# Optimization experiments

Hardware: AMD Instinct MI355X
Metric: run time of the kernel (lower is better)

The kernel has to match this reference:

```python
import jax, jax.numpy as jnp
import numpy as np

B, S, D, H = 4, 1024, 512, 8
DH = D // H
INNER = 1536  # int(2*D*4/3) rounded up to multiple of 256


def setup_inputs() -> dict:
    key = jax.random.key(0)
    ks = jax.random.split(key, 16)
    g = lambda i, shape, fan: (jax.random.normal(ks[i], shape, jnp.float32) / np.sqrt(fan))
    return {
        "x": jax.random.normal(ks[0], (B, S, D), jnp.float32),
        "Wq": g(1, (D, D), D), "bq": jnp.zeros((D,), jnp.float32),
        "Wkv": g(2, (D, 2 * D), D), "bkv": jnp.zeros((2 * D,), jnp.float32),
        "Wo": g(3, (D, D), D), "bo": jnp.zeros((D,), jnp.float32),
        "rms_w": jnp.ones((D,), jnp.float32),
        "l1": g(4, (D, INNER), D), "l2": g(5, (D, INNER), D), "l3": g(6, (INNER, D), INNER),
        "in_w": jnp.ones((D,), jnp.float32), "in_b": jnp.zeros((D,), jnp.float32),
    }


def rms_norm(x, w, eps=1e-6):
    return x * jax.lax.rsqrt(jnp.mean(x * x, axis=-1, keepdims=True) + eps) * w


def instance_norm(x, w, b, eps=1e-5):
    # InstanceNorm1d(affine=True) over the sequence dim per (batch, channel); x: [B,S,D]
    m = jnp.mean(x, axis=1, keepdims=True)
    v = jnp.mean((x - m) ** 2, axis=1, keepdims=True)
    return (x - m) * jax.lax.rsqrt(v + eps) * w + b


def sparse_sdpa(q, k, v):
    # q,k,v: [B,H,S,DH]
    b, h, s, dh = q.shape
    scores = jnp.einsum("bhsd,bhtd->bhst", q, k) / np.sqrt(dh).astype(np.float32)
    w = jax.nn.softmax(scores, axis=-1)
    kk = s // 2
    _, idx = jax.lax.top_k(w, kk)  # [B,H,S,kk]
    bi = jnp.arange(b)[:, None, None, None]
    hi = jnp.arange(h)[None, :, None, None]
    ri = jnp.arange(s)[None, None, :, None]
    mask = jnp.zeros_like(w).at[bi, hi, ri, idx].set(1.0)
    masked = jnp.where(mask > 0, w, 0.0)  # zeros (not -inf), per original
    aw = jax.nn.softmax(masked, axis=-1)
    return jnp.einsum("bhst,bhtd->bhsd", aw, v)


def reference(x, Wq, bq, Wkv, bkv, Wo, bo, rms_w, l1, l2, l3, in_w, in_b):
    # attention: q from Wq, k/v from packed Wkv ('b s (two h d)')
    q = (x @ Wq + bq).reshape(B, S, H, DH).transpose(0, 2, 1, 3)
    kv = (x @ Wkv + bkv).reshape(B, S, 2, H, DH)
    k = kv[:, :, 0].transpose(0, 2, 1, 3)
    v = kv[:, :, 1].transpose(0, 2, 1, 3)
    o = sparse_sdpa(q, k, v)
    attn_out = o.transpose(0, 2, 1, 3).reshape(B, S, D) @ Wo + bo
    h_hat = rms_norm(x + attn_out, rms_w)
    ffn = (jax.nn.silu(h_hat @ l1) * (h_hat @ l2)) @ l3
    return instance_norm(h_hat + ffn, in_w, in_b)
```

## Files before the change

kernel.cpp:

```cpp
#include <hip/hip_runtime.h>
#include <stdint.h>

#define B_ 4
#define S_ 1024
#define D_ 512
#define H_ 8
#define DH_ 64
#define INNER_ 1536
#define M_ (B_*S_)

typedef unsigned short u16;
typedef __attribute__((ext_vector_type(8))) short sh8;
typedef __attribute__((ext_vector_type(8))) _Float16 h8;
typedef __attribute__((ext_vector_type(4))) _Float16 h4;
typedef __attribute__((ext_vector_type(2))) _Float16 h2f;
typedef __attribute__((ext_vector_type(4))) float f32x4;

typedef __attribute__((address_space(1))) const void cgv;
typedef __attribute__((address_space(3))) void lv;
__device__ __forceinline__ void gl_lds16(const void* g, void* l) {
  __builtin_amdgcn_global_load_lds((cgv*)g, (lv*)l, 16, 0, 0);
}
#define WAITVM(N) __builtin_amdgcn_s_waitcnt(0x0F70 | (N))

__device__ __forceinline__ float bf2f(u16 u) {
  union { unsigned int i; float f; } v; v.i = ((unsigned int)u) << 16; return v.f;
}
__device__ __forceinline__ u16 f2bf(float f) {
  union { float f; unsigned int i; } v; v.f = f;
  unsigned int u = v.i;
  return (u16)((u + 0x7FFFu + ((u >> 16) & 1u)) >> 16);
}
__device__ __forceinline__ u16 f2h(float f) {
  _Float16 h = (_Float16)f;
  return *(u16*)&h;
}

__global__ __launch_bounds__(256) void prep_all(
    const float* __restrict__ Wq, const float* __restrict__ Wkv,
    const float* __restrict__ Wo, const float* __restrict__ l1,
    const float* __restrict__ l2, const float* __restrict__ l3,
    const float* __restrict__ x,
    u16* __restrict__ Wt1, u16* __restrict__ Wot,
    u16* __restrict__ W12t, u16* __restrict__ l3t,
    u16* __restrict__ xb)
{
  int i = blockIdx.x;
  if (i >= 832) {
    int e = ((i - 832) * 256 + threadIdx.x) * 4;
    float4 v = *(const float4*)(x + e);
    uint2 o;
    o.x = (unsigned int)f2bf(v.x) | ((unsigned int)f2bf(v.y) << 16);
    o.y = (unsigned int)f2bf(v.z) | ((unsigned int)f2bf(v.w) << 16);
    *(uint2*)(xb + e) = o;
    return;
  }
  const float* in; u16* outp; int K, N, bx, by, rs = 1, ra = 0;
  if (i < 64)       { in = Wq;  outp = Wt1;              K = 512;  N = 512;           bx = i & 7;  by = i >> 3; }
  else if (i < 192) { in = Wkv; outp = Wt1 + 512 * 512;  K = 512;  N = 1024; i -= 64; bx = i & 15; by = i >> 4; }
  else if (i < 256) { in = Wo;  outp = Wot;              K = 512;  N = 512;  i -= 192; bx = i & 7;  by = i >> 3; }
  else if (i < 448) { in = l1;  outp = W12t;             K = 512;  N = 1536; i -= 256; bx = i % 24; by = i / 24; rs = 2; ra = 0; }
  else if (i < 640) { in = l2;  outp = W12t;             K = 512;  N = 1536; i -= 448; bx = i % 24; by = i / 24; rs = 2; ra = 1; }
  else              { in = l3;  outp = l3t;              K = 1536; N = 512;  i -= 640; bx = i & 7;  by = i >> 3; }

  __shared__ u16 tile[64][65];
  int tx = threadIdx.x & 63, ty = threadIdx.x >> 6;
  int n0 = bx * 64, k0 = by * 64;
  #pragma unroll
  for (int t = 0; t < 16; t++) {
    int k = ty + t * 4;
    tile[k][tx] = f2bf(in[(size_t)(k0 + k) * N + n0 + tx]);
  }
  __syncthreads();
  #pragma unroll
  for (int t = 0; t < 16; t++) {
    int n = ty + t * 4;
    outp[(size_t)((n0 + n) * rs + ra) * K + k0 + tx] = tile[tx][n];
  }
}

template<int EPI>
__global__ __launch_bounds__(256) void gemm_bt(
    const u16* __restrict__ A, const u16* __restrict__ Bt,
    int M, int N, int K,
    const float* __restrict__ bias0, const float* __restrict__ bias1,
    u16* __restrict__ outU,
    u16* __restrict__ qo, u16* __restrict__ ko_, u16* __restrict__ vto)
{
  __shared__ u16 As[2 * 128 * 32];
  __shared__ u16 Bs[2 * 128 * 32];
  int tid = threadIdx.x;
  int gx = blockIdx.x, gy = blockIdx.y;
  int l = tid & 63, w = tid >> 6;
  int l15 = l & 15, quad = l >> 4;
  int wm = (w >> 1) * 64, wn = (w & 1) * 64;
  f32x4 acc[4][4] = {};

  const u16* Ag = A  + (size_t)(gy * 128 + (tid >> 2)) * K + (tid & 3) * 8;
  const u16* Bg = Bt + (size_t)(gx * 128 + (tid >> 2)) * K + (tid & 3) * 8;

  gl_lds16(Ag,                  &As[tid * 8]);
  gl_lds16(Ag + (size_t)64 * K, &As[2048 + tid * 8]);
  gl_lds16(Bg,                  &Bs[tid * 8]);
  gl_lds16(Bg + (size_t)64 * K, &Bs[2048 + tid * 8]);
  __syncthreads();

  int cur = 0;
  for (int ko = 0; ko < K; ko += 32) {
    int nxt = cur ^ 1;
    if (ko + 32 < K) {
      gl_lds16(Ag + ko + 32,                  &As[nxt * 4096 + tid * 8]);
      gl_lds16(Ag + (size_t)64 * K + ko + 32, &As[nxt * 4096 + 2048 + tid * 8]);
      gl_lds16(Bg + ko + 32,                  &Bs[nxt * 4096 + tid * 8]);
      gl_lds16(Bg + (size_t)64 * K + ko + 32, &Bs[nxt * 4096 + 2048 + tid * 8]);
    }
    int base = cur * 4096;
    sh8 af[4], bfr[4];
    #pragma unroll
    for (int mi = 0; mi < 4; mi++)
      af[mi] = *(const sh8*)&As[base + (wm + mi * 16 + l15) * 32 + quad * 8];
    #pragma unroll
    for (int ni = 0; ni < 4; ni++)
      bfr[ni] = *(const sh8*)&Bs[base + (wn + ni * 16 + l15) * 32 + quad * 8];
    #pragma unroll
    for (int mi = 0; mi < 4; mi++)
      #pragma unroll
      for (int ni = 0; ni < 4; ni++)
        acc[mi][ni] = __builtin_amdgcn_mfma_f32_16x16x32_bf16(af[mi], bfr[ni], acc[mi][ni], 0, 0, 0);
    __syncthreads();
    cur = nxt;
  }

  #pragma unroll
  for (int mi = 0; mi < 4; mi++) {
    #pragma unroll
    for (int ni = 0; ni < 4; ni++) {
      #pragma unroll
      for (int r = 0; r < 4; r++) {
        int grow = gy * 128 + wm + mi * 16 + quad * 4 + r;
        int gcol = gx * 128 + wn + ni * 16 + l15;
        float v = acc[mi][ni][r];
        if (EPI == 1) {
          int b = grow >> 10, s = grow & 1023;
          if (gcol < 512) {
            int h = gcol >> 6, dh = gcol & 63;
            qo[(((size_t)b * H_ + h) * S_ + s) * DH_ + dh] = f2h(v + bias0[gcol]);
          } else {
            int n2 = gcol - 512;
            int two = n2 >> 9, h = (n2 >> 6) & 7, dh = n2 & 63;
            float vv = v + bias1[n2];
            if (two == 0) ko_[(((size_t)b * H_ + h) * S_ + s) * DH_ + dh] = f2h(vv);
            else          vto[(((size_t)b * H_ + h) * DH_ + dh) * S_ + s] = f2h(vv);
          }
        } else {
          float vp = __shfl_xor(v, 1);
          if ((l15 & 1) == 0) {
            float a = v, b = vp;
            float gv = a / (1.f + __expf(-a)) * b;
            outU[(size_t)grow * (N >> 1) + (gcol >> 1)] = f2bf(gv);
          }
        }
      }
    }
  }
}

template<int EPI>
__global__ __launch_bounds__(256) void gemm_n64(
    const u16* __restrict__ A, const u16* __restrict__ Bt,
    int M, int N, int K,
    const float* __restrict__ bias0, const float* __restrict__ auxF,
    const u16* __restrict__ auxH, float* __restrict__ outF,
    float* __restrict__ part)
{
  __shared__ u16 sbuf[4 * 3 * 3072];
  __shared__ float ss1[4][2][16], ss2[4][2][16];
  int tid = threadIdx.x;
  int gx = blockIdx.x, gy = blockIdx.y;
  int l = tid & 63, w = tid >> 6;
  int l15 = l & 15, quad = l >> 4;
  int wm = (w >> 1) * 64, wn = (w & 1) * 32;
  int lr = l >> 2, lc = l & 3;
  f32x4 acc[4][2] = {};

  u16* wb = sbuf + (size_t)w * (3 * 3072);
  const u16* Aw = A  + (size_t)(gy * 128 + wm + lr) * K + lc * 8;
  const u16* Bw = Bt + (size_t)(gx * 64  + wn + lr) * K + lc * 8;

  auto stage = [&](int t, int buf) {
    u16* d = wb + buf * 3072;
    const u16* a = Aw + t * 32;
    gl_lds16(a,                  d + l * 8);
    gl_lds16(a + (size_t)16 * K, d + 512  + l * 8);
    gl_lds16(a + (size_t)32 * K, d + 1024 + l * 8);
    gl_lds16(a + (size_t)48 * K, d + 1536 + l * 8);
    const u16* b2 = Bw + t * 32;
    gl_lds16(b2,                  d + 2048 + l * 8);
    gl_lds16(b2 + (size_t)16 * K, d + 2560 + l * 8);
  };

  int nT = K >> 5;
  stage(0, 0);
  stage(1, 1);
  int cb = 0;
  for (int t = 0; t < nT; t++) {
    int nb = (cb == 2) ? 0 : cb + 1;
    int pb = (nb == 2) ? 0 : nb + 1;
    if (t + 2 < nT)      { stage(t + 2, pb); WAITVM(12); }
    else if (t + 1 < nT) { WAITVM(6); }
    else                 { WAITVM(0); }
    const u16* d = wb + cb * 3072;
    sh8 af[4], bfr[2];
    #pragma unroll
    for (int mi = 0; mi < 4; mi++)
      af[mi] = *(const sh8*)&d[(mi * 16 + l15) * 32 + quad * 8];
    #pragma unroll
    for (int ni = 0; ni < 2; ni++)
      bfr[ni] = *(const sh8*)&d[2048 + (ni * 16 + l15) * 32 + quad * 8];
    #pragma unroll
    for (int mi = 0; mi < 4; mi++)
      #pragma unroll
      for (int ni = 0; ni < 2; ni++)
        acc[mi][ni] = __builtin_amdgcn_mfma_f32_16x16x32_bf16(af[mi], bfr[ni], acc[mi][ni], 0, 0, 0);
    cb = nb;
  }

  float cs1[2] = {0.f, 0.f}, cs2[2] = {0.f, 0.f};
  #pragma unroll
  for (int mi = 0; mi < 4; mi++) {
    #pragma unroll
    for (int ni = 0; ni < 2; ni++) {
      #pragma unroll
      for (int r = 0; r < 4; r++) {
        int grow = gy * 128 + wm + mi * 16 + quad * 4 + r;
        int gcol = gx * 64 + wn + ni * 16 + l15;
        float v = acc[mi][ni][r];
        if (EPI == 2) v += bias0[gcol] + auxF[(size_t)grow * N + gcol];
        else          v += bf2f(auxH[(size_t)grow * N + gcol]);
        outF[(size_t)grow * N + gcol] = v;
        if (EPI == 4) { cs1[ni] += v; cs2[ni] += v * v; }
      }
    }
  }
  if (EPI == 4) {
    #pragma unroll
    for (int ni = 0; ni < 2; ni++) {
      cs1[ni] += __shfl_xor(cs1[ni], 16); cs1[ni] += __shfl_xor(cs1[ni], 32);
      cs2[ni] += __shfl_xor(cs2[ni], 16); cs2[ni] += __shfl_xor(cs2[ni], 32);
    }
    if (l < 16) {
      ss1[w][0][l15] = cs1[0]; ss1[w][1][l15] = cs1[1];
      ss2[w][0][l15] = cs2[0]; ss2[w][1][l15] = cs2[1];
    }
    __syncthreads();
    if (tid < 64) {
      int wsel = (tid >> 5) & 1, ni = (tid >> 4) & 1, cl = tid & 15;
      float s1 = ss1[wsel][ni][cl] + ss1[wsel + 2][ni][cl];
      float s2 = ss2[wsel][ni][cl] + ss2[wsel + 2][ni][cl];
      int col = gx * 64 + wsel * 32 + ni * 16 + cl;
      int b = gy >> 3, seg = gy & 7;
      float2 p; p.x = s1; p.y = s2;
      *(float2*)&part[((size_t)(b * 512 + col) * 8 + seg) * 2] = p;
    }
  }
}

#define RSTRIDE 1032
#define STAGE_H (16 * RSTRIDE)
__global__ __launch_bounds__(256, 3) void attn_kernel(
    const u16* __restrict__ q, const u16* __restrict__ kk,
    const u16* __restrict__ vt, u16* __restrict__ attn)
{
  __shared__ u16 scb[16 * RSTRIDE + 4 * 2048 + 256];
  float* sums = (float*)(scb + 16 * RSTRIDE + 4 * 2048);

  int tid = threadIdx.x;
  int l = tid & 63, w = tid >> 6;
  int l15 = l & 15, quad = l >> 4;
  int blk = blockIdx.x;
  int xcd = blk & 7, li = blk >> 3;
  int bh = xcd * 4 + (li & 3);
  int r0 = (li >> 2) << 4;

  const u16* qb = q  + ((size_t)bh * S_ + r0) * DH_;
  const u16* kb = kk + (size_t)bh * S_ * DH_;
  const u16* vb = vt + (size_t)bh * DH_ * S_;

  int ws = STAGE_H + w * 2048;
  int lr = l >> 2, lc = l & 3;

  {
    const u16* s0 = kb + (size_t)((w << 4) + lr) * DH_ + lc * 8;
    gl_lds16(s0,      &scb[ws + l * 8]);
    gl_lds16(s0 + 32, &scb[ws + 512 + l * 8]);
    const u16* s1 = kb + (size_t)(((1 << 6) | (w << 4)) + lr) * DH_ + lc * 8;
    gl_lds16(s1,      &scb[ws + 1024 + l * 8]);
    gl_lds16(s1 + 32, &scb[ws + 1536 + l * 8]);
  }

  h8 aq0 = *(const h8*)(qb + l15 * DH_ + quad * 8);
  h8 aq1 = *(const h8*)(qb + l15 * DH_ + 32 + quad * 8);

  uint32_t kv[32];
  float S1 = 0.f, S2 = 0.f;
  #pragma unroll
  for (int i = 0; i < 16; i++) {
    if (i + 2 < 16) {
      int t0n = (((i + 2) << 2) | w) << 4;
      const u16* src = kb + (size_t)(t0n + lr) * DH_ + lc * 8;
      int sb = ws + ((i + 2) & 1) * 1024;
      gl_lds16(src,      &scb[sb + l * 8]);
      gl_lds16(src + 32, &scb[sb + 512 + l * 8]);
    }
    if (i + 2 < 16) { WAITVM(4); } else if (i + 1 < 16) { WAITVM(2); } else { WAITVM(0); }
    int sb = ws + (i & 1) * 1024;
    h8 bk0 = *(const h8*)&scb[sb + l15 * 32 + quad * 8];
    h8 bk1 = *(const h8*)&scb[sb + 512 + l15 * 32 + quad * 8];
    f32x4 s4 = {};
    s4 = __builtin_amdgcn_mfma_f32_16x16x32_f16(bk0, aq0, s4, 0, 0, 0);
    s4 = __builtin_amdgcn_mfma_f32_16x16x32_f16(bk1, aq1, s4, 0, 0, 0);
    float e0 = exp2f(fmaf(s4[0], 0.18033688f, -11.5415603f));
    float e1 = exp2f(fmaf(s4[1], 0.18033688f, -11.5415603f));
    float e2 = exp2f(fmaf(s4[2], 0.18033688f, -11.5415603f));
    float e3 = exp2f(fmaf(s4[3], 0.18033688f, -11.5415603f));
    S1 += e0 + e1 + e2 + e3;
    S2 += e0 * e0 + e1 * e1 + e2 * e2 + e3 * e3;
    h2f p0; p0[0] = (_Float16)e0; p0[1] = (_Float16)e1;
    h2f p1; p1[0] = (_Float16)e2; p1[1] = (_Float16)e3;
    kv[2 * i]     = __builtin_bit_cast(uint32_t, p0);
    kv[2 * i + 1] = __builtin_bit_cast(uint32_t, p1);
  }
  S1 += __shfl_xor(S1, 16); S1 += __shfl_xor(S1, 32);
  S2 += __shfl_xor(S2, 16); S2 += __shfl_xor(S2, 32);
  if (l < 16) {
    sums[(w * 16 + l15) * 2]     = S1;
    sums[(w * 16 + l15) * 2 + 1] = S2;
  }
  __syncthreads();

  int n0 = w << 4;
  const u16* vsrc = vb + (size_t)(n0 + lr) * S_ + lc * 8;
  gl_lds16(vsrc,      &scb[ws + l * 8]);
  gl_lds16(vsrc + 32, &scb[ws + 512 + l * 8]);
  gl_lds16(vsrc + 64, &scb[ws + 1024 + l * 8]);

  float Z1 = 0.f, S2t = 0.f;
  #pragma unroll
  for (int ww = 0; ww < 4; ww++) {
    Z1  += sums[(ww * 16 + l15) * 2];
    S2t += sums[(ww * 16 + l15) * 2 + 1];
  }
  float invZ1 = 1.0f / Z1;
  float Z2 = 1025.0f + 0.5f * S2t * invZ1 * invZ1;
  float invZ2 = 1.0f / Z2;

  _Float16 izh = (_Float16)invZ1;
  h2f izv; izv[0] = izh; izv[1] = izh;
  _Float16 z2h = (_Float16)invZ2;
  h2f z2v; z2v[0] = z2h; z2v[1] = z2h;
  h2f onev; onev[0] = (_Float16)1.f; onev[1] = (_Float16)1.f;
  h2f c2v;  c2v[0] = (_Float16)0.5f; c2v[1] = (_Float16)0.5f;
  h2f c6v;  c6v[0] = (_Float16)(1.f/6.f); c6v[1] = (_Float16)(1.f/6.f);
  #pragma unroll
  for (int i = 0; i < 16; i++) {
    int t0 = ((i << 2) | w) << 4;
    uint2 ov;
    #pragma unroll
    for (int hwd = 0; hwd < 2; hwd++) {
      h2f e = __builtin_bit_cast(h2f, kv[2 * i + hwd]);
      h2f wv = e * izv;
      h2f p = wv * c6v + c2v;
      h2f qq = wv * p + onev;
      h2f cm1 = wv * qq;
      h2f cp = cm1 * z2v + z2v;
      (&ov.x)[hwd] = __builtin_bit_cast(uint32_t, cp);
    }
    *(uint2*)(scb + l15 * RSTRIDE + t0 + quad * 4) = ov;
  }
  __syncthreads();

  const u16* crow = scb + l15 * RSTRIDE;
  f32x4 oacc = {};
  #pragma unroll
  for (int kt = 0; kt < 32; kt++) {
    if (kt + 3 < 32)
      gl_lds16(vsrc + (kt + 3) * 32, &scb[ws + ((kt + 3) & 3) * 512 + l * 8]);
    if (kt < 29) { WAITVM(3); } else if (kt == 29) { WAITVM(2); }
    else if (kt == 30) { WAITVM(1); } else { WAITVM(0); }
    h8 ca = *(const h8*)(crow + kt * 32 + quad * 8);
    h8 vv = *(const h8*)&scb[ws + (kt & 3) * 512 + l15 * 32 + quad * 8];
    oacc = __builtin_amdgcn_mfma_f32_16x16x32_f16(ca, vv, oacc, 0, 0, 0);
  }
  int b = bh >> 3, hh = bh & 7;
  #pragma unroll
  for (int r = 0; r < 4; r++) {
    int rr = quad * 4 + r;
    attn[((size_t)b * S_ + r0 + rr) * D_ + hh * DH_ + n0 + l15] = f2bf(oacc[r]);
  }
}

__global__ __launch_bounds__(128) void rms_kernel(const float* __restrict__ in,
                                                  const float* __restrict__ w,
                                                  u16* __restrict__ out) {
  int row = blockIdx.x;
  int tid = threadIdx.x;
  const float* r = in + (size_t)row * D_;
  float v0 = r[tid], v1 = r[tid + 128], v2 = r[tid + 256], v3 = r[tid + 384];
  float s = v0 * v0 + v1 * v1 + v2 * v2 + v3 * v3;
  #pragma unroll
  for (int d = 1; d < 64; d <<= 1) s += __shfl_xor(s, d);
  __shared__ float red[2];
  if ((tid & 63) == 0) red[tid >> 6] = s;
  __syncthreads();
  s = red[0] + red[1];
  float rs = rsqrtf(s * (1.0f / 512.0f) + 1e-6f);
  out[(size_t)row * D_ + tid      ] = f2bf(v0 * rs * w[tid      ]);
  out[(size_t)row * D_ + tid + 128] = f2bf(v1 * rs * w[tid + 128]);
  out[(size_t)row * D_ + tid + 256] = f2bf(v2 * rs * w[tid + 256]);
  out[(size_t)row * D_ + tid + 384] = f2bf(v3 * rs * w[tid + 384]);
}

__global__ __launch_bounds__(256) void inorm_stats2(const float* __restrict__ part,
                                                    float* __restrict__ stats) {
  int idx = blockIdx.x * 256 + threadIdx.x;
  float s1 = 0.f, s2 = 0.f;
  #pragma unroll
  for (int i = 0; i < 8; i++) {
    float2 p = *(const float2*)&part[((size_t)idx * 8 + i) * 2];
    s1 += p.x; s2 += p.y;
  }
  float m = s1 * (1.f / 1024.f);
  float var = s2 * (1.f / 1024.f) - m * m;
  stats[idx * 2]     = m;
  stats[idx * 2 + 1] = rsqrtf(var + 1e-5f);
}

__global__ __launch_bounds__(256) void inorm_apply(const float* __restrict__ y,
                                                   const float* __restrict__ stats,
                                                   const float* __restrict__ w,
                                                   const float* __restrict__ bias,
                                                   float* __restrict__ out) {
  int row = blockIdx.x;
  int b = row >> 10;
  int tid = threadIdx.x;
  #pragma unroll
  for (int i = 0; i < 2; i++) {
    int d = tid + i * 256;
    float m  = stats[((size_t)b * D_ + d) * 2];
    float rs = stats[((size_t)b * D_ + d) * 2 + 1];
    float v = y[(size_t)row * D_ + d];
    out[(size_t)row * D_ + d] = (v - m) * rs * w[d] + bias[d];
  }
}

extern "C" void kernel_launch(void* const* d_in, const int* in_sizes, int n_in,
                              void* d_out, int out_size, void* d_ws, size_t ws_size,
                              hipStream_t stream) {
  const float* x    = (const float*)d_in[0];
  const float* Wq   = (const float*)d_in[1];
  const float* bq   = (const float*)d_in[2];
  const float* Wkv  = (const float*)d_in[3];
  const float* bkv  = (const float*)d_in[4];
  const float* Wo   = (const float*)d_in[5];
  const float* bo   = (const float*)d_in[6];
  const float* rmsw = (const float*)d_in[7];
  const float* l1   = (const float*)d_in[8];
  const float* l2   = (const float*)d_in[9];
  const float* l3   = (const float*)d_in[10];
  const float* inw  = (const float*)d_in[11];
  const float* inb  = (const float*)d_in[12];
  float* out = (float*)d_out;

  char* ws = (char*)d_ws;
  size_t off = 0;
  auto alloc = [&](size_t n) { char* p = ws + off; off += (n + 255) & ~(size_t)255; return p; };
  u16*  xb   = (u16*) alloc((size_t)M_ * D_ * 2);
  u16*  Wt1  = (u16*) alloc((size_t)1536 * 512 * 2);
  u16*  Wot  = (u16*) alloc((size_t)512 * 512 * 2);
  u16*  W12t = (u16*) alloc((size_t)3072 * 512 * 2);
  u16*  l3t  = (u16*) alloc((size_t)512 * 1536 * 2);
  u16*  qb   = (u16*) alloc((size_t)M_ * D_ * 2);
  u16*  kb   = (u16*) alloc((size_t)M_ * D_ * 2);
  u16*  vtb  = (u16*) alloc((size_t)M_ * D_ * 2);
  u16*  attn = (u16*) alloc((size_t)M_ * D_ * 2);
  float* tmpF = (float*)alloc((size_t)M_ * D_ * 4);
  u16*  hhat = (u16*) alloc((size_t)M_ * D_ * 2);
  u16*  g    = (u16*) alloc((size_t)M_ * INNER_ * 2);
  float* part  = (float*)alloc((size_t)B_ * D_ * 8 * 2 * 4);
  float* stats = (float*)alloc((size_t)B_ * D_ * 2 * 4);

  prep_all<<<2880, 256, 0, stream>>>(Wq, Wkv, Wo, l1, l2, l3, x,
                                     Wt1, Wot, W12t, l3t, xb);

  gemm_bt<1><<<dim3(12, 32), 256, 0, stream>>>(xb, Wt1, M_, 1536, 512,
      bq, bkv, nullptr, qb, kb, vtb);

  attn_kernel<<<2048, 256, 0, stream>>>(qb, kb, vtb, attn);

  gemm_n64<2><<<dim3(8, 32), 256, 0, stream>>>(attn, Wot, M_, 512, 512,
      bo, x, nullptr, tmpF, nullptr);

  rms_kernel<<<4096, 128, 0, stream>>>(tmpF, rmsw, hhat);

  gemm_bt<3><<<dim3(24, 32), 256, 0, stream>>>(hhat, W12t, M_, 3072, 512,
      nullptr, nullptr, g, nullptr, nullptr, nullptr);

  gemm_n64<4><<<dim3(8, 32), 256, 0, stream>>>(g, l3t, M_, 512, 1536,
      nullptr, nullptr, hhat, tmpF, part);

  inorm_stats2<<<8, 256, 0, stream>>>(part, stats);
  inorm_apply<<<4096, 256, 0, stream>>>(tmpF, stats, inw, inb, out);
}
```

Measured before the change: 220.8 us.

## Triple-buffer GEMM LDS pipeline with vmcnt waits; vectorize weight transpose stores

The bf16 GEMM moves from double to triple buffering of LDS tiles, so loads run two stages ahead. Explicit vmcnt waits with raw s_barrier replace __syncthreads, letting the next stage's loads stay in flight across the barrier. Launch bounds now request 3 blocks per CU, and the weight-transpose kernel writes packed 32-bit pairs instead of 16-bit stores. The extra LDS buffer (48KB per block) may limit occupancy, and the hand-written waitcnt logic risks ordering mistakes.

```diff
diff --git a/kernel.cpp b/kernel.cpp
--- a/kernel.cpp
+++ b/kernel.cpp
@@ -73,22 +73,24 @@
   }
   __syncthreads();
   #pragma unroll
-  for (int t = 0; t < 16; t++) {
-    int n = ty + t * 4;
-    outp[(size_t)((n0 + n) * rs + ra) * K + k0 + tx] = tile[tx][n];
+  for (int t = 0; t < 8; t++) {
+    int n = (threadIdx.x >> 5) + t * 8;
+    int c = (threadIdx.x & 31) * 2;
+    unsigned int val = (unsigned int)tile[c][n] | ((unsigned int)tile[c + 1][n] << 16);
+    *(unsigned int*)&outp[(size_t)((n0 + n) * rs + ra) * K + k0 + c] = val;
   }
 }
 
 template<int EPI>
-__global__ __launch_bounds__(256) void gemm_bt(
+__global__ __launch_bounds__(256, 3) void gemm_bt(
     const u16* __restrict__ A, const u16* __restrict__ Bt,
     int M, int N, int K,
     const float* __restrict__ bias0, const float* __restrict__ bias1,
     u16* __restrict__ outU,
     u16* __restrict__ qo, u16* __restrict__ ko_, u16* __restrict__ vto)
 {
-  __shared__ u16 As[2 * 128 * 32];
-  __shared__ u16 Bs[2 * 128 * 32];
+  __shared__ u16 As[3 * 128 * 32];
+  __shared__ u16 Bs[3 * 128 * 32];
   int tid = threadIdx.x;
   int gx = blockIdx.x, gy = blockIdx.y;
   int l = tid & 63, w = tid >> 6;
@@ -99,22 +101,28 @@
   const u16* Ag = A  + (size_t)(gy * 128 + (tid >> 2)) * K + (tid & 3) * 8;
   const u16* Bg = Bt + (size_t)(gx * 128 + (tid >> 2)) * K + (tid & 3) * 8;
 
-  gl_lds16(Ag,                  &As[tid * 8]);
-  gl_lds16(Ag + (size_t)64 * K, &As[2048 + tid * 8]);
-  gl_lds16(Bg,                  &Bs[tid * 8]);
-  gl_lds16(Bg + (size_t)64 * K, &Bs[2048 + tid * 8]);
-  __syncthreads();
-
-  int cur = 0;
-  for (int ko = 0; ko < K; ko += 32) {
-    int nxt = cur ^ 1;
-    if (ko + 32 < K) {
-      gl_lds16(Ag + ko + 32,                  &As[nxt * 4096 + tid * 8]);
-      gl_lds16(Ag + (size_t)64 * K + ko + 32, &As[nxt * 4096 + 2048 + tid * 8]);
-      gl_lds16(Bg + ko + 32,                  &Bs[nxt * 4096 + tid * 8]);
-      gl_lds16(Bg + (size_t)64 * K + ko + 32, &Bs[nxt * 4096 + 2048 + tid * 8]);
-    }
-    int base = cur * 4096;
+  auto stage = [&](int t2, int buf) {
+    int ko2 = t2 * 32;
+    gl_lds16(Ag + ko2,                  &As[buf * 4096 + tid * 8]);
+    gl_lds16(Ag + (size_t)64 * K + ko2, &As[buf * 4096 + 2048 + tid * 8]);
+    gl_lds16(Bg + ko2,                  &Bs[buf * 4096 + tid * 8]);
+    gl_lds16(Bg + (size_t)64 * K + ko2, &Bs[buf * 4096 + 2048 + tid * 8]);
+  };
+
+  const int nT = K >> 5;
+  stage(0, 0);
+  stage(1, 1);
+  WAITVM(4);
+  __builtin_amdgcn_s_barrier();
+  __builtin_amdgcn_sched_barrier(0);
+
+  int cb = 0;
+  for (int t = 0; t < nT; t++) {
+    if (t + 2 < nT) {
+      int pb = cb + 2; if (pb >= 3) pb -= 3;
+      stage(t + 2, pb);
+    }
+    int base = cb * 4096;
     sh8 af[4], bfr[4];
     #pragma unroll
     for (int mi = 0; mi < 4; mi++)
@@ -127,8 +135,14 @@
       #pragma unroll
       for (int ni = 0; ni < 4; ni++)
         acc[mi][ni] = __builtin_amdgcn_mfma_f32_16x16x32_bf16(af[mi], bfr[ni], acc[mi][ni], 0, 0, 0);
-    __syncthreads();
-    cur = nxt;
+    __builtin_amdgcn_sched_barrier(0);
+    if (t + 1 < nT) {
+      if (t + 2 < nT) { WAITVM(4); }
+      else            { WAITVM(0); }
+      __builtin_amdgcn_s_barrier();
+      __builtin_amdgcn_sched_barrier(0);
+    }
+    cb++; if (cb >= 3) cb -= 3;
   }
 
   #pragma unroll
```

After: 221.9 us. No clear change (+0.5%).
